# Kernel tuning notes

Measured on AMD Instinct MI355X. Metric: run time of the kernel, lower is better.

The kernel has to match this reference:

```python
import jax, jax.numpy as jnp
import numpy as np

ALPHA = 0.25
GAMMA = 2.0
CLS_EPS = 1e-4


def _make_boxes(key, n, img=512.0, smin=32.0, smax=128.0, yx=False):
    k1, k2, k3, k4 = jax.random.split(key, 4)
    cx = jax.random.uniform(k1, (n,)) * img
    cy = jax.random.uniform(k2, (n,)) * img
    w = smin + jax.random.uniform(k3, (n,)) * (smax - smin)
    h = smin + jax.random.uniform(k4, (n,)) * (smax - smin)
    if yx:  # anchor format (y1, x1, y2, x2)
        return jnp.stack([cy - h / 2, cx - w / 2, cy + h / 2, cx + w / 2], axis=1)
    # annotation format (x1, y1, x2, y2)
    return jnp.stack([cx - w / 2, cy - h / 2, cx + w / 2, cy + h / 2], axis=1)


def setup_inputs() -> dict:
    key = jax.random.key(0)
    B, A, C, M = 4, 100000, 80, 32
    k = jax.random.split(key, 6)
    classifications = jax.random.uniform(k[0], (B, A, C), dtype=jnp.float32)
    regressions = jax.random.normal(k[1], (B, A, 7), dtype=jnp.float32)
    anchors = _make_boxes(k[2], A, yx=True)[None]  # [1, A, 4] (y1,x1,y2,x2)
    boxes = jax.vmap(lambda kk: _make_boxes(kk, M))(jax.random.split(k[3], B))  # [B, M, 4]
    labels = jax.random.randint(k[4], (B, M), 0, C).astype(jnp.float32)
    annotations = jnp.concatenate([boxes, labels[..., None]], axis=-1)  # [B, M, 5]
    return {"classifications": classifications, "regressions": regressions,
            "anchors": anchors, "annotations": annotations}


def reference(classifications, regressions, anchors, annotations):
    B, A, C = classifications.shape
    anchor = anchors[0]  # [A, 4] (y1, x1, y2, x2)
    aw = anchor[:, 3] - anchor[:, 1]
    ah = anchor[:, 2] - anchor[:, 0]
    acx = anchor[:, 1] + 0.5 * aw
    acy = anchor[:, 0] + 0.5 * ah
    area_a = (anchor[:, 2] - anchor[:, 0]) * (anchor[:, 3] - anchor[:, 1])

    def per_image(cls, reg, ann):
        M_ = ann.shape[0]
        b = ann[:, :4]  # (x1, y1, x2, y2)
        labels = ann[:, 4].astype(jnp.int32)
        cls = jnp.clip(cls, CLS_EPS, 1.0 - CLS_EPS)
        # IoU [A, M] (same axis convention as calc_iou)
        iw = jnp.clip(jnp.minimum(anchor[:, 3:4], b[None, :, 2]) - jnp.maximum(anchor[:, 1:2], b[None, :, 0]), 0.0)
        ih = jnp.clip(jnp.minimum(anchor[:, 2:3], b[None, :, 3]) - jnp.maximum(anchor[:, 0:1], b[None, :, 1]), 0.0)
        area_b = (b[:, 2] - b[:, 0]) * (b[:, 3] - b[:, 1])
        inter = iw * ih
        ua = jnp.clip(area_a[:, None] + area_b[None, :] - inter, 1e-8)
        iou = inter / ua
        iou_max = iou.max(axis=1)
        iou_argmax = iou.argmax(axis=1)  # [A]
        pos = iou_max >= 0.5
        neg = iou_max < 0.4
        num_pos = pos.sum()
        posf = pos.astype(cls.dtype)
        # classification targets: -1 ignore, 0 background, one-hot positives
        assigned_box = b[iou_argmax]           # [A, 4]
        assigned_lbl = labels[iou_argmax]      # [A]
        onehot = jax.nn.one_hot(assigned_lbl, C, dtype=cls.dtype)
        tgt = jnp.where(pos[:, None], onehot, jnp.where(neg[:, None], 0.0, -1.0))
        alpha_f = jnp.where(tgt == 1.0, ALPHA, 1.0 - ALPHA)
        focal_w = alpha_f * jnp.where(tgt == 1.0, 1.0 - cls, cls) ** GAMMA
        bce = -(tgt * jnp.log(cls) + (1.0 - tgt) * jnp.log(1.0 - cls))
        cls_loss = jnp.where(tgt != -1.0, focal_w * bce, 0.0).sum() / jnp.maximum(num_pos.astype(cls.dtype), 1.0)
        gw = assigned_box[:, 2] - assigned_box[:, 0]
        gh = assigned_box[:, 3] - assigned_box[:, 1]
        gcx = assigned_box[:, 0] + 0.5 * gw
        gcy = assigned_box[:, 1] + 0.5 * gh
        gw = jnp.clip(gw, 1.0)
        gh = jnp.clip(gh, 1.0)
        rt = jnp.stack([(gcy - acy) / ah, (gcx - acx) / aw,
                        jnp.log(gh / ah), jnp.log(gw / aw)], axis=1)  # [A, 4] (dy,dx,dh,dw)
        diff = jnp.abs(rt - reg[:, :4])
        sl1 = jnp.where(diff <= 1.0 / 9.0, 0.5 * 9.0 * diff ** 2, diff - 0.5 / 9.0)
        reg_loss = (sl1 * posf[:, None]).sum() / jnp.maximum(num_pos * 4, 1).astype(cls.dtype)
        # embedding grouping loss (segment mean per GT box over positive anchors)
        emb = reg[:, 4:7]
        counts = jax.ops.segment_sum(posf, iou_argmax, num_segments=M_)          # [M]
        sums = jax.ops.segment_sum(emb * posf[:, None], iou_argmax, num_segments=M_)  # [M, 3]
        mean = jnp.where((counts > 0)[:, None], sums / jnp.maximum(counts, 1.0)[:, None], 0.0)
        mdet = jax.lax.stop_gradient(mean)
        sq = jax.ops.segment_sum((((emb - mdet[iou_argmax]) ** 2).sum(-1)) * posf, iou_argmax, num_segments=M_)
        per_ann = jnp.where(counts > 0, sq / jnp.maximum(counts * 3.0, 1.0), 0.0)
        emb_loss = per_ann.sum() / M_
        return cls_loss, reg_loss, emb_loss, mean

    cls_l, reg_l, emb_l, embs = jax.vmap(per_image)(classifications, regressions, annotations)
    losses = jnp.stack([cls_l.mean(), reg_l.mean() * 50.0, emb_l.mean()])
    return losses, embs
```

## Files before the change

kernel.cpp:

```cpp
#include <hip/hip_runtime.h>

#define CLS_LO 1.0e-4f
#define CLS_HI 0.9999f


__device__ __forceinline__ float smooth_l1(float d) {
    d = fabsf(d);
    return (d <= (1.0f / 9.0f)) ? (4.5f * d * d) : (d - (0.5f / 9.0f));
}

__global__ void __launch_bounds__(256)
det_assign_kernel(const float* __restrict__ cls,
                  const float* __restrict__ reg,
                  const float* __restrict__ anc,
                  const float* __restrict__ ann,
                  float* __restrict__ ws,
                  float* __restrict__ maskf,
                  int A, int C, int M)
{
    const int b   = blockIdx.y;
    const int tid = threadIdx.x;
    const int a   = blockIdx.x * 256 + tid;
    const int S   = 5 * M + 192;

    __shared__ float4 sbox[64];
    __shared__ float  slbl[64];
    __shared__ float  s_cnt[64], s_sx[64], s_sy[64], s_sz[64], s_sq[64];
    __shared__ float  s_part[4][3];

    if (tid < M) {
        const float* bp = ann + ((size_t)b * M + tid) * 5;
        sbox[tid] = make_float4(bp[0], bp[1], bp[2], bp[3]);
        slbl[tid] = bp[4];
        s_cnt[tid] = 0.f; s_sx[tid] = 0.f; s_sy[tid] = 0.f; s_sz[tid] = 0.f; s_sq[tid] = 0.f;
    }
    __syncthreads();

    float contrib_cls = 0.f, contrib_reg = 0.f, contrib_np = 0.f;

    if (a < A) {
        float4 av = ((const float4*)anc)[a];
        const float ay1 = av.x, ax1 = av.y, ay2 = av.z, ax2 = av.w;
        const float aw  = ax2 - ax1;
        const float ah  = ay2 - ay1;
        const float area_a = ah * aw;

        float best = -1.0f;
        int   bj   = 0;
#define IOU_BODY(j)                                                              \
        {                                                                        \
            const float4 bx = sbox[(j)];                                         \
            float iw = fminf(ax2, bx.z) - fmaxf(ax1, bx.x); iw = fmaxf(iw, 0.f); \
            float ih = fminf(ay2, bx.w) - fmaxf(ay1, bx.y); ih = fmaxf(ih, 0.f); \
            const float inter = iw * ih;                                         \
            const float ua = fmaxf(area_a + (bx.z - bx.x) * (bx.w - bx.y)        \
                                   - inter, 1e-8f);                              \
            const float iou = inter / ua;                                        \
            if (iou > best) { best = iou; bj = (j); }                            \
        }
        if (M == 32) {
            #pragma unroll
            for (int j = 0; j < 32; j++) IOU_BODY(j)
        } else {
            for (int j = 0; j < M; j++) IOU_BODY(j)
        }
#undef IOU_BODY
        const bool pos = best >= 0.5f;
        const bool neg = best < 0.4f;
        maskf[(size_t)b * A + a] = (pos || neg) ? 1.f : 0.f;

        if (pos) {
            contrib_np = 1.0f;

            const float* cbase = cls + ((size_t)b * A + a) * (size_t)C;
            const int L = (int)slbl[bj];
            const float p = fminf(fmaxf(cbase[L], CLS_LO), CLS_HI);
            contrib_cls = 0.25f * (1.f - p) * (1.f - p) * (-__logf(p))
                        - 0.75f * p * p * (-__logf(1.f - p));

            const float* rp = reg + ((size_t)b * A + a) * 7;
            const float r0 = rp[0], r1 = rp[1], r2 = rp[2], r3 = rp[3];
            const float e0 = rp[4], e1 = rp[5], e2 = rp[6];

            const float4 bx = sbox[bj];
            float gw = bx.z - bx.x;
            float gh = bx.w - bx.y;
            const float gcx = bx.x + 0.5f * gw;
            const float gcy = bx.y + 0.5f * gh;
            gw = fmaxf(gw, 1.f);
            gh = fmaxf(gh, 1.f);
            const float acx = ax1 + 0.5f * aw;
            const float acy = ay1 + 0.5f * ah;
            contrib_reg = smooth_l1((gcy - acy) / ah - r0) +
                          smooth_l1((gcx - acx) / aw - r1) +
                          smooth_l1(logf(gh / ah) - r2) +
                          smooth_l1(logf(gw / aw) - r3);

            atomicAdd(&s_cnt[bj], 1.f);
            atomicAdd(&s_sx[bj], e0);
            atomicAdd(&s_sy[bj], e1);
            atomicAdd(&s_sz[bj], e2);
            atomicAdd(&s_sq[bj], e0 * e0 + e1 * e1 + e2 * e2);
        }
    }

    for (int off = 32; off > 0; off >>= 1) {
        contrib_cls += __shfl_down(contrib_cls, off, 64);
        contrib_reg += __shfl_down(contrib_reg, off, 64);
        contrib_np  += __shfl_down(contrib_np,  off, 64);
    }
    if ((tid & 63) == 0) {
        s_part[tid >> 6][0] = contrib_cls;
        s_part[tid >> 6][1] = contrib_reg;
        s_part[tid >> 6][2] = contrib_np;
    }
    __syncthreads();

    float* wsb = ws + (size_t)b * S;
    if (tid < M) {
        const float c = s_cnt[tid];
        if (c != 0.f) {
            atomicAdd(&wsb[tid], c);
            atomicAdd(&wsb[M + 3 * tid + 0], s_sx[tid]);
            atomicAdd(&wsb[M + 3 * tid + 1], s_sy[tid]);
            atomicAdd(&wsb[M + 3 * tid + 2], s_sz[tid]);
            atomicAdd(&wsb[4 * M + tid], s_sq[tid]);
        }
    }
    if (tid == 0) {
        const float c = s_part[0][0] + s_part[1][0] + s_part[2][0] + s_part[3][0];
        const float r = s_part[0][1] + s_part[1][1] + s_part[2][1] + s_part[3][1];
        const float n = s_part[0][2] + s_part[1][2] + s_part[2][2] + s_part[3][2];
        float* slot = wsb + 5 * M + 3 * (blockIdx.x & 63);
        if (c != 0.f) atomicAdd(&slot[0], c);
        if (r != 0.f) atomicAdd(&slot[1], r);
        if (n != 0.f) atomicAdd(&slot[2], n);
    }
}

template <int CPA4>
__global__ void __launch_bounds__(256, 6)
det_focal_kernel(const float* __restrict__ cls,
                 const float* __restrict__ maskf,
                 float* __restrict__ ws,
                 int A, int C, int M)
{
    const int b     = blockIdx.y;
    const int aBase = blockIdx.x * 128;
    const int tid   = threadIdx.x;
    const int S     = 5 * M + 192;
    const int cpa4  = CPA4 ? CPA4 : (C >> 2);

    __shared__ float smask[128];
    if (tid < 128) {
        const int a = aBase + tid;
        smask[tid] = (a < A) ? maskf[(size_t)b * A + a] : 0.f;
    }
    __syncthreads();

    const int nA = min(128, A - aBase);
    const float4* tile = (const float4*)(cls + ((size_t)b * A + aBase) * (size_t)C);
    float acc = 0.f;

    if (CPA4 == 20 && nA == 128) {
        float4 v[10];
        #pragma unroll
        for (int k = 0; k < 10; k++)
            v[k] = tile[tid + 256 * k];
        float m[10];
        #pragma unroll
        for (int k = 0; k < 10; k++)
            m[k] = smask[(((unsigned)tid + 256u * k) * 52429u) >> 20];
        #pragma unroll
        for (int k = 0; k < 10; k++) {
            float p, l, s = 0.f;
            p = fminf(fmaxf(v[k].x, CLS_LO), CLS_HI); l = __logf(1.f - p); s = fmaf(p * p, l, s);
            p = fminf(fmaxf(v[k].y, CLS_LO), CLS_HI); l = __logf(1.f - p); s = fmaf(p * p, l, s);
            p = fminf(fmaxf(v[k].z, CLS_LO), CLS_HI); l = __logf(1.f - p); s = fmaf(p * p, l, s);
            p = fminf(fmaxf(v[k].w, CLS_LO), CLS_HI); l = __logf(1.f - p); s = fmaf(p * p, l, s);
            acc = fmaf(m[k], s, acc);
        }
    } else {
        const int n4 = nA * cpa4;
        for (int idx = tid; idx < n4; idx += 256) {
            const float m = smask[(unsigned)idx / (unsigned)cpa4];
            const float4 vv = tile[idx];
            float p, l, s = 0.f;
            p = fminf(fmaxf(vv.x, CLS_LO), CLS_HI); l = __logf(1.f - p); s = fmaf(p * p, l, s);
            p = fminf(fmaxf(vv.y, CLS_LO), CLS_HI); l = __logf(1.f - p); s = fmaf(p * p, l, s);
            p = fminf(fmaxf(vv.z, CLS_LO), CLS_HI); l = __logf(1.f - p); s = fmaf(p * p, l, s);
            p = fminf(fmaxf(vv.w, CLS_LO), CLS_HI); l = __logf(1.f - p); s = fmaf(p * p, l, s);
            acc = fmaf(m, s, acc);
        }
    }

    for (int off = 32; off > 0; off >>= 1)
        acc += __shfl_down(acc, off, 64);
    __shared__ float sp[4];
    if ((tid & 63) == 0) sp[tid >> 6] = acc;
    __syncthreads();
    if (tid == 0) {
        const float tot = sp[0] + sp[1] + sp[2] + sp[3];
        atomicAdd(&ws[(size_t)b * S + 5 * M + 3 * (blockIdx.x & 63) + 0], -0.75f * tot);
    }
}

__global__ void __launch_bounds__(256)
det_final_kernel(const float* __restrict__ ws,
                 float* __restrict__ out,
                 int B, int M)
{
    const int t = threadIdx.x;
    const int S = 5 * M + 192;
    __shared__ float s_scal[8][3];
    __shared__ float s_emb[8];
    if (t < B) s_emb[t] = 0.f;

    const int k = t & 63;
    for (int b = t >> 6; b < B; b += 4) {
        const float* slot = ws + (size_t)b * S + 5 * M + 3 * k;
        float c = slot[0], r = slot[1], n = slot[2];
        for (int off = 32; off > 0; off >>= 1) {
            c += __shfl_down(c, off, 64);
            r += __shfl_down(r, off, 64);
            n += __shfl_down(n, off, 64);
        }
        if (k == 0) { s_scal[b][0] = c; s_scal[b][1] = r; s_scal[b][2] = n; }
    }
    __syncthreads();

    if (t < B * M) {
        const int b = t / M;
        const int m = t - b * M;
        const float* wsb = ws + (size_t)b * S;
        const float c = wsb[m];
        float mx = 0.f, my = 0.f, mz = 0.f, pa = 0.f;
        if (c > 0.f) {
            mx = wsb[M + 3 * m + 0] / c;
            my = wsb[M + 3 * m + 1] / c;
            mz = wsb[M + 3 * m + 2] / c;
            const float sq = wsb[4 * M + m] - c * (mx * mx + my * my + mz * mz);
            pa = sq / fmaxf(c * 3.f, 1.f);
        }
        out[3 + (size_t)(b * M + m) * 3 + 0] = mx;
        out[3 + (size_t)(b * M + m) * 3 + 1] = my;
        out[3 + (size_t)(b * M + m) * 3 + 2] = mz;
        atomicAdd(&s_emb[b], pa);
    }
    __syncthreads();

    if (t == 0) {
        float cl = 0.f, rl = 0.f, el = 0.f;
        for (int b = 0; b < B; b++) {
            const float np = s_scal[b][2];
            cl += s_scal[b][0] / fmaxf(np, 1.f);
            rl += s_scal[b][1] / fmaxf(4.f * np, 1.f);
            el += s_emb[b] / (float)M;
        }
        const float invB = 1.f / (float)B;
        out[0] = cl * invB;
        out[1] = rl * invB * 50.f;
        out[2] = el * invB;
    }
}

extern "C" void kernel_launch(void* const* d_in, const int* in_sizes, int n_in,
                              void* d_out, int out_size, void* d_ws, size_t ws_size,
                              hipStream_t stream) {
    const float* cls = (const float*)d_in[0];
    const float* reg = (const float*)d_in[1];
    const float* anc = (const float*)d_in[2];
    const float* ann = (const float*)d_in[3];
    float* out = (float*)d_out;
    float* ws  = (float*)d_ws;

    const int A = in_sizes[2] / 4;
    const int B = in_sizes[1] / (A * 7);
    const int C = in_sizes[0] / (B * A);
    const int M = in_sizes[3] / (B * 5);
    const int S = 5 * M + 192;
    float* maskf = ws + (size_t)B * S;

    hipMemsetAsync(ws, 0, (size_t)B * S * sizeof(float), stream);

    dim3 gridA((A + 255) / 256, B);
    det_assign_kernel<<<gridA, 256, 0, stream>>>(cls, reg, anc, ann, ws, maskf, A, C, M);

    dim3 gridB((A + 127) / 128, B);
    if (C == 80)
        det_focal_kernel<20><<<gridB, 256, 0, stream>>>(cls, maskf, ws, A, C, M);
    else
        det_focal_kernel<0><<<gridB, 256, 0, stream>>>(cls, maskf, ws, A, C, M);

    det_final_kernel<<<1, 256, 0, stream>>>(ws, out, B, M);
}
```

Baseline: 242.5 us.

## Stage focal-loss tiles via direct global-to-LDS loads and drop IoU division

The focal kernel now processes 64 anchors per block and loads each 64x80 class tile straight into shared memory with global_load_lds before computing, in place of holding ten float4 loads per thread in registers. Making the load asynchronous is meant to cut register pressure and raise occupancy while the stream stays bandwidth bound. The IoU argmax in the assign kernel compares cross-multiplied fractions instead of dividing, and the pos/neg thresholds are tested the same way. The regression log uses the fast __logf intrinsic. The fraction compare can break near-ties differently than the reference, and the tile costs 20 KB of LDS per block.

New measurement: 241.3 us. No clear change (-0.5%).

```diff
diff --git a/kernel.cpp b/kernel.cpp
--- a/kernel.cpp
+++ b/kernel.cpp
@@ -45,8 +45,8 @@
         const float ah  = ay2 - ay1;
         const float area_a = ah * aw;
 
-        float best = -1.0f;
-        int   bj   = 0;
+        float bN = -1.f, bD = 1.f;
+        int   bj = 0;
 #define IOU_BODY(j)                                                              \
         {                                                                        \
             const float4 bx = sbox[(j)];                                         \
@@ -55,8 +55,7 @@
             const float inter = iw * ih;                                         \
             const float ua = fmaxf(area_a + (bx.z - bx.x) * (bx.w - bx.y)        \
                                    - inter, 1e-8f);                              \
-            const float iou = inter / ua;                                        \
-            if (iou > best) { best = iou; bj = (j); }                            \
+            if (inter * bD > bN * ua) { bN = inter; bD = ua; bj = (j); }         \
         }
         if (M == 32) {
             #pragma unroll
@@ -65,8 +64,8 @@
             for (int j = 0; j < M; j++) IOU_BODY(j)
         }
 #undef IOU_BODY
-        const bool pos = best >= 0.5f;
-        const bool neg = best < 0.4f;
+        const bool pos = (2.f * bN >= bD);
+        const bool neg = (bN < 0.4f * bD);
         maskf[(size_t)b * A + a] = (pos || neg) ? 1.f : 0.f;
 
         if (pos) {
@@ -93,8 +92,8 @@
             const float acy = ay1 + 0.5f * ah;
             contrib_reg = smooth_l1((gcy - acy) / ah - r0) +
                           smooth_l1((gcx - acx) / aw - r1) +
-                          smooth_l1(logf(gh / ah) - r2) +
-                          smooth_l1(logf(gw / aw) - r3);
+                          smooth_l1(__logf(gh / ah) - r2) +
+                          smooth_l1(__logf(gw / aw) - r3);
 
             atomicAdd(&s_cnt[bj], 1.f);
             atomicAdd(&s_sx[bj], e0);
@@ -138,53 +137,62 @@
     }
 }
 
+typedef const __attribute__((address_space(1))) unsigned int ga_u32;
+typedef __attribute__((address_space(3))) unsigned int ls_u32;
+
 template <int CPA4>
-__global__ void __launch_bounds__(256, 6)
+__global__ void __launch_bounds__(256)
 det_focal_kernel(const float* __restrict__ cls,
                  const float* __restrict__ maskf,
                  float* __restrict__ ws,
                  int A, int C, int M)
 {
     const int b     = blockIdx.y;
-    const int aBase = blockIdx.x * 128;
+    const int aBase = blockIdx.x * 64;
     const int tid   = threadIdx.x;
     const int S     = 5 * M + 192;
     const int cpa4  = CPA4 ? CPA4 : (C >> 2);
 
-    __shared__ float smask[128];
-    if (tid < 128) {
-        const int a = aBase + tid;
-        smask[tid] = (a < A) ? maskf[(size_t)b * A + a] : 0.f;
-    }
-    __syncthreads();
-
-    const int nA = min(128, A - aBase);
-    const float4* tile = (const float4*)(cls + ((size_t)b * A + aBase) * (size_t)C);
+    __shared__ float tile[64 * 80];
+    __shared__ float smask[64];
+
+    const int nA = min(64, A - aBase);
+    const float* gtile = cls + ((size_t)b * A + aBase) * (size_t)C;
     float acc = 0.f;
 
-    if (CPA4 == 20 && nA == 128) {
-        float4 v[10];
+    if (CPA4 == 20 && nA == 64) {
+        const int wave = tid >> 6;
+        const int lane = tid & 63;
         #pragma unroll
-        for (int k = 0; k < 10; k++)
-            v[k] = tile[tid + 256 * k];
-        float m[10];
+        for (int k = 0; k < 5; k++) {
+            const int f4 = wave * 320 + k * 64 + lane;
+            const float* g = gtile + 4 * f4;
+            float* l = tile + 4 * (wave * 320 + k * 64);
+            __builtin_amdgcn_global_load_lds((ga_u32*)g, (ls_u32*)l, 16, 0, 0);
+        }
+        if (tid < 64) smask[tid] = maskf[(size_t)b * A + aBase + tid];
+        __builtin_amdgcn_s_waitcnt(0);
+        __syncthreads();
+
         #pragma unroll
-        for (int k = 0; k < 10; k++)
-            m[k] = smask[(((unsigned)tid + 256u * k) * 52429u) >> 20];
-        #pragma unroll
-        for (int k = 0; k < 10; k++) {
+        for (int k = 0; k < 5; k++) {
+            const unsigned idx = (unsigned)tid + 256u * k;
+            const float4 v = ((const float4*)tile)[idx];
+            const float m = smask[(idx * 52429u) >> 20];
             float p, l, s = 0.f;
-            p = fminf(fmaxf(v[k].x, CLS_LO), CLS_HI); l = __logf(1.f - p); s = fmaf(p * p, l, s);
-            p = fminf(fmaxf(v[k].y, CLS_LO), CLS_HI); l = __logf(1.f - p); s = fmaf(p * p, l, s);
-            p = fminf(fmaxf(v[k].z, CLS_LO), CLS_HI); l = __logf(1.f - p); s = fmaf(p * p, l, s);
-            p = fminf(fmaxf(v[k].w, CLS_LO), CLS_HI); l = __logf(1.f - p); s = fmaf(p * p, l, s);
-            acc = fmaf(m[k], s, acc);
+            p = fminf(fmaxf(v.x, CLS_LO), CLS_HI); l = __logf(1.f - p); s = fmaf(p * p, l, s);
+            p = fminf(fmaxf(v.y, CLS_LO), CLS_HI); l = __logf(1.f - p); s = fmaf(p * p, l, s);
+            p = fminf(fmaxf(v.z, CLS_LO), CLS_HI); l = __logf(1.f - p); s = fmaf(p * p, l, s);
+            p = fminf(fmaxf(v.w, CLS_LO), CLS_HI); l = __logf(1.f - p); s = fmaf(p * p, l, s);
+            acc = fmaf(m, s, acc);
         }
     } else {
+        if (tid < 64) smask[tid] = (aBase + tid < A) ? maskf[(size_t)b * A + aBase + tid] : 0.f;
+        __syncthreads();
         const int n4 = nA * cpa4;
         for (int idx = tid; idx < n4; idx += 256) {
             const float m = smask[(unsigned)idx / (unsigned)cpa4];
-            const float4 vv = tile[idx];
+            const float4 vv = ((const float4*)gtile)[idx];
             float p, l, s = 0.f;
             p = fminf(fmaxf(vv.x, CLS_LO), CLS_HI); l = __logf(1.f - p); s = fmaf(p * p, l, s);
             p = fminf(fmaxf(vv.y, CLS_LO), CLS_HI); l = __logf(1.f - p); s = fmaf(p * p, l, s);
@@ -286,7 +294,7 @@
     dim3 gridA((A + 255) / 256, B);
     det_assign_kernel<<<gridA, 256, 0, stream>>>(cls, reg, anc, ann, ws, maskf, A, C, M);
 
-    dim3 gridB((A + 127) / 128, B);
+    dim3 gridB((A + 63) / 64, B);
     if (C == 80)
         det_focal_kernel<20><<<gridB, 256, 0, stream>>>(cls, maskf, ws, A, C, M);
     else
```
